# Performance work log

Hardware: AMD Instinct MI355X
Metric: run time of the kernel (lower is better)

Reference implementation:

```python
import jax, jax.numpy as jnp
import numpy as np

N = 50000      # nodes
E = 800000     # edges (before self loops)
D_IN = 128
HID = 64
HEADS = 8
D_OUT = 10


def setup_inputs() -> dict:
    key = jax.random.key(0)
    ks = jax.random.split(key, 16)
    sc = 0.05
    x = jax.random.normal(ks[0], (N, D_IN), dtype=jnp.float32)
    edge_index = jax.random.randint(ks[1], (2, E), 0, N, dtype=jnp.int64)
    return {
        "x": x,
        "edge_index": edge_index,
        "W1": jax.random.normal(ks[2], (HEADS * HID, D_IN), dtype=jnp.float32) * sc,
        "a1_src": jax.random.normal(ks[3], (HEADS, HID), dtype=jnp.float32) * sc,
        "a1_dst": jax.random.normal(ks[4], (HEADS, HID), dtype=jnp.float32) * sc,
        "b1": jnp.zeros((HEADS * HID,), jnp.float32),
        "W2": jax.random.normal(ks[5], (HID, HEADS * HID), dtype=jnp.float32) * sc,
        "a2_src": jax.random.normal(ks[6], (1, HID), dtype=jnp.float32) * sc,
        "a2_dst": jax.random.normal(ks[7], (1, HID), dtype=jnp.float32) * sc,
        "b2": jnp.zeros((HID,), jnp.float32),
        "W3": jax.random.normal(ks[8], (HID, HID), dtype=jnp.float32) * sc,
        "a3_src": jax.random.normal(ks[9], (1, HID), dtype=jnp.float32) * sc,
        "a3_dst": jax.random.normal(ks[10], (1, HID), dtype=jnp.float32) * sc,
        "b3": jnp.zeros((HID,), jnp.float32),
        "Wc": jax.random.normal(ks[11], (D_OUT, HID), dtype=jnp.float32) * sc,
        "bc": jnp.zeros((D_OUT,), jnp.float32),
    }


def gat_conv(x, src, dst, W, a_src, a_dst, b, concat):
    """PyG GATConv (eval mode, add_self_loops already applied to src/dst)."""
    heads, out_ch = a_src.shape
    n = x.shape[0]
    h = (x @ W.T).reshape(n, heads, out_ch)          # [N, H, C]
    a_s = jnp.einsum('nhc,hc->nh', h, a_src)          # [N, H]
    a_d = jnp.einsum('nhc,hc->nh', h, a_dst)          # [N, H]
    e = jax.nn.leaky_relu(a_s[src] + a_d[dst], 0.2)   # [Etot, H]
    # segment softmax over incoming edges of each destination node
    m = jax.ops.segment_max(e, dst, num_segments=n)
    ex = jnp.exp(e - m[dst])
    s = jax.ops.segment_sum(ex, dst, num_segments=n)
    alpha = ex / (s[dst] + 1e-16)                     # [Etot, H]
    out = jax.ops.segment_sum(h[src] * alpha[:, :, None], dst, num_segments=n)
    if concat:
        out = out.reshape(n, heads * out_ch)
    else:
        out = out.mean(axis=1)
    return out + b


def reference(x, edge_index, W1, a1_src, a1_dst, b1, W2, a2_src, a2_dst, b2,
              W3, a3_src, a3_dst, b3, Wc, bc):
    loops = jnp.arange(N, dtype=edge_index.dtype)
    src = jnp.concatenate([edge_index[0], loops])
    dst = jnp.concatenate([edge_index[1], loops])
    h = jax.nn.elu(gat_conv(x, src, dst, W1, a1_src, a1_dst, b1, True))
    h = jax.nn.elu(gat_conv(h, src, dst, W2, a2_src, a2_dst, b2, False))
    h = jax.nn.elu(gat_conv(h, src, dst, W3, a3_src, a3_dst, b3, False))
    return h @ Wc.T + bc
```

## Files before the change

### kernel.cpp

```cpp
#include <hip/hip_runtime.h>
#include <math.h>

#define N_NODES 50000
#define N_EDGES 800000
#define ETOT    (N_EDGES + N_NODES)
#define COL_CAP (ETOT + 3 * N_NODES + 64)

typedef short bf16x8 __attribute__((ext_vector_type(8)));
typedef float f32x4  __attribute__((ext_vector_type(4)));
typedef float f32x2  __attribute__((ext_vector_type(2)));

__device__ __forceinline__ float b2f(unsigned int u16) {
    return __uint_as_float(u16 << 16);
}
__device__ __forceinline__ unsigned short f2b(float f) {
    unsigned int u = __float_as_uint(f);
    u += 0x7fffu + ((u >> 16) & 1u);
    return (unsigned short)(u >> 16);
}

__global__ __launch_bounds__(256) void k_prep(const float* __restrict__ x,
                                              const float* __restrict__ w1,
                                              const float* __restrict__ w2,
                                              const float* __restrict__ w3,
                                              const float* __restrict__ a1s,
                                              const float* __restrict__ a1d,
                                              unsigned short* __restrict__ xb,
                                              unsigned short* __restrict__ o1,
                                              unsigned short* __restrict__ o2,
                                              unsigned short* __restrict__ o3,
                                              float* __restrict__ U,
                                              int* __restrict__ deg,
                                              int* __restrict__ flag) {
    int i = blockIdx.x * 256 + threadIdx.x;
    if (i < N_NODES) deg[i] = 0;
    if (i == 0) *flag = 0;
    if (blockIdx.x < 8) {
        int h = blockIdx.x;
        int which = threadIdx.x >> 7, k = threadIdx.x & 127;
        const float* av = which ? a1d : a1s;
        float acc = 0.f;
        for (int c = 0; c < 64; ++c)
            acc += av[h * 64 + c] * w1[(size_t)(h * 64 + c) * 128 + k];
        U[(which * 8 + h) * 128 + k] = acc;
    }
    if (i < 512 * 128 / 4) {
        float4 v = ((const float4*)w1)[i];
        ushort2* o = (ushort2*)(o1 + i * 4);
        o[0] = make_ushort2(f2b(v.x), f2b(v.y));
        o[1] = make_ushort2(f2b(v.z), f2b(v.w));
    }
    if (i < 64 * 512 / 4) {
        float4 v = ((const float4*)w2)[i];
        ushort2* o = (ushort2*)(o2 + i * 4);
        o[0] = make_ushort2(f2b(v.x), f2b(v.y));
        o[1] = make_ushort2(f2b(v.z), f2b(v.w));
    }
    if (i < 64 * 64 / 4) {
        float4 v = ((const float4*)w3)[i];
        ushort2* o = (ushort2*)(o3 + i * 4);
        o[0] = make_ushort2(f2b(v.x), f2b(v.y));
        o[1] = make_ushort2(f2b(v.z), f2b(v.w));
    }
    if (i < N_NODES * 128 / 8) {
        const float4* xp = (const float4*)x + (size_t)i * 2;
        float4 v0 = xp[0], v1 = xp[1];
        unsigned int u0 = (unsigned int)f2b(v0.x) | ((unsigned int)f2b(v0.y) << 16);
        unsigned int u1 = (unsigned int)f2b(v0.z) | ((unsigned int)f2b(v0.w) << 16);
        unsigned int u2 = (unsigned int)f2b(v1.x) | ((unsigned int)f2b(v1.y) << 16);
        unsigned int u3 = (unsigned int)f2b(v1.z) | ((unsigned int)f2b(v1.w) << 16);
        *(uint4*)(xb + (size_t)i * 8) = make_uint4(u0, u1, u2, u3);
    }
}

__global__ __launch_bounds__(256) void k_attn(const unsigned short* __restrict__ xb,
                                              const float* __restrict__ U,
                                              float* __restrict__ asrc,
                                              float* __restrict__ adst) {
    __shared__ float sU[16 * 132];
    __shared__ unsigned short sX[16 * 136];
    int t = threadIdx.x;
    for (int i = t; i < 2048; i += 256) sU[(i >> 7) * 132 + (i & 127)] = U[i];
    int n0 = blockIdx.x * 16;
    {
        int r = t >> 4, c = (t & 15) * 8;
        *(uint4*)&sX[r * 136 + c] = *(const uint4*)(xb + (size_t)(n0 + r) * 128 + c);
    }
    __syncthreads();
    int nl = t >> 4, o = t & 15;
    const unsigned short* xr = sX + nl * 136;
    const float* ur = sU + o * 132;
    float acc = 0.f;
#pragma unroll 8
    for (int k2 = 0; k2 < 128; ++k2) acc += b2f(xr[k2]) * ur[k2];
    int n = n0 + nl;
    if (o < 8) asrc[n * 8 + o] = acc;
    else       adst[n * 8 + (o - 8)] = acc;
}

__global__ void k_detect(const int* __restrict__ idx, int* __restrict__ flag) {
    int i = blockIdx.x * blockDim.x + threadIdx.x;
    int v = idx[2 * i + 1];
    unsigned long long any = __ballot(v != 0);
    if ((threadIdx.x & 63) == 0 && any) atomicOr(flag, 1);
}

__device__ __forceinline__ int edge_src(const int* idx, int e, int is32) {
    return is32 ? idx[e] : idx[2 * e];
}
__device__ __forceinline__ int edge_dst(const int* idx, int e, int is32) {
    return is32 ? idx[N_EDGES + e] : idx[2 * (N_EDGES + e)];
}

__global__ void k_degree(const int* __restrict__ idx, const int* __restrict__ flag,
                         int* __restrict__ deg) {
    int e = blockIdx.x * blockDim.x + threadIdx.x;
    if (e >= ETOT) return;
    int is32 = *flag;
    int d = (e < N_EDGES) ? edge_dst(idx, e, is32) : (e - N_EDGES);
    atomicAdd(&deg[d], 1);
}

__global__ __launch_bounds__(256) void k_scan1(const int* __restrict__ deg,
                                               int* __restrict__ rowptr,
                                               int* __restrict__ bsum) {
    __shared__ int sd[256];
    int t = threadIdx.x;
    int i = blockIdx.x * 256 + t;
    int v = (i < N_NODES) ? ((deg[i] + 3) & ~3) : 0;
    sd[t] = v;
    __syncthreads();
#pragma unroll
    for (int off = 1; off < 256; off <<= 1) {
        int a = (t >= off) ? sd[t - off] : 0;
        __syncthreads();
        sd[t] += a;
        __syncthreads();
    }
    if (i < N_NODES) rowptr[i] = sd[t] - v;
    if (t == 255) bsum[blockIdx.x] = sd[255];
}

__global__ __launch_bounds__(256) void k_scan2(int* __restrict__ bsum,
                                               int* __restrict__ boff,
                                               int* __restrict__ rowptr,
                                               int nb) {
    __shared__ int sd[256];
    int t = threadIdx.x;
    int v = (t < nb) ? bsum[t] : 0;
    sd[t] = v;
    __syncthreads();
#pragma unroll
    for (int off = 1; off < 256; off <<= 1) {
        int a = (t >= off) ? sd[t - off] : 0;
        __syncthreads();
        sd[t] += a;
        __syncthreads();
    }
    boff[t] = sd[t] - v;
    if (t == 255) rowptr[N_NODES] = sd[255];
}

__global__ __launch_bounds__(256) void k_scan3(int* __restrict__ rowptr,
                                               const int* __restrict__ boff,
                                               const int* __restrict__ deg,
                                               int* __restrict__ cursor,
                                               int* __restrict__ col) {
    int i = blockIdx.x * 256 + threadIdx.x;
    if (i == 0) {
        int tot = rowptr[N_NODES];
        for (int q = 0; q < 48; ++q) col[tot + q] = 0;
    }
    if (i >= N_NODES) return;
    int r = rowptr[i] + boff[blockIdx.x];
    rowptr[i] = r;
    cursor[i] = r;
    int d = deg[i];
    int pd = (d + 3) & ~3;
    for (int p = r + d; p < r + pd; ++p) col[p] = 0;
}

__global__ void k_scatter(const int* __restrict__ idx, const int* __restrict__ flag,
                          int* __restrict__ cursor, int* __restrict__ col) {
    int e = blockIdx.x * blockDim.x + threadIdx.x;
    if (e >= ETOT) return;
    int is32 = *flag;
    int s, d;
    if (e < N_EDGES) { s = edge_src(idx, e, is32); d = edge_dst(idx, e, is32); }
    else             { s = d = e - N_EDGES; }
    int pos = atomicAdd(&cursor[d], 1);
    col[pos] = s;
}

__device__ __forceinline__ void aggx_slot(int idx, int rem, float tt, unsigned int xx,
                                          float adn, float& ssum, f32x2* acc) {
    float e = tt + adn;
    e = fmaxf(e, 0.2f * e);
    float ex = __expf(e);
    ex = (idx < rem) ? ex : 0.f;
    ssum += ex;
    float fx = __uint_as_float(xx << 16);
    float fy = __uint_as_float(xx & 0xffff0000u);
    int exi = __float_as_int(ex);
#pragma unroll
    for (int hh = 0; hh < 8; ++hh) {
        float wh = __int_as_float(__builtin_amdgcn_readlane(exi, hh << 3));
        acc[hh].x = fmaf(fx, wh, acc[hh].x);
        acc[hh].y = fmaf(fy, wh, acc[hh].y);
    }
}

__global__ __launch_bounds__(256) void k_aggx(const unsigned short* __restrict__ xb,
                                              const float* __restrict__ asrc,
                                              const float* __restrict__ adst,
                                              const int* __restrict__ rowptr,
                                              const int* __restrict__ degv,
                                              const int* __restrict__ col,
                                              unsigned short* __restrict__ aggX) {
    int n = blockIdx.x * 4 + (threadIdx.x >> 6);
    if (n >= N_NODES) return;
    int l = threadIdx.x & 63;
    int j = l >> 3;
    unsigned lx2 = (unsigned)(l << 1);
    int start = rowptr[n];
    int end   = start + degv[n];
    float adn = adst[((unsigned)n << 3) + (unsigned)j];

    float ssum = 0.f;
    f32x2 acc[8];
#pragma unroll
    for (int hh = 0; hh < 8; ++hh) acc[hh] = (f32x2){0.f, 0.f};

    float tA0, tA1, tA2, tA3, tB0, tB1, tB2, tB3;
    unsigned int xA0, xA1, xA2, xA3, xB0, xB1, xB2, xB3;
    int4 cA, cB;

#define GATHX(c, T0, T1, T2, T3, X0, X1, X2, X3)                              \
    T0 = asrc[(((unsigned)(c).x) << 3) + (unsigned)j];                        \
    T1 = asrc[(((unsigned)(c).y) << 3) + (unsigned)j];                        \
    T2 = asrc[(((unsigned)(c).z) << 3) + (unsigned)j];                        \
    T3 = asrc[(((unsigned)(c).w) << 3) + (unsigned)j];                        \
    X0 = *(const unsigned int*)(xb + (((unsigned)(c).x) << 7) + lx2);         \
    X1 = *(const unsigned int*)(xb + (((unsigned)(c).y) << 7) + lx2);         \
    X2 = *(const unsigned int*)(xb + (((unsigned)(c).z) << 7) + lx2);         \
    X3 = *(const unsigned int*)(xb + (((unsigned)(c).w) << 7) + lx2);

    int k = start;
    cA = *(const int4*)(col + k);
    cB = *(const int4*)(col + k + 4);
    GATHX(cA, tA0, tA1, tA2, tA3, xA0, xA1, xA2, xA3);
    for (;;) {
        bool hasB = (k + 4 < end);
        if (hasB) {
            GATHX(cB, tB0, tB1, tB2, tB3, xB0, xB1, xB2, xB3);
            cA = *(const int4*)(col + k + 8);
        }
        {
            int rem = end - k;
            aggx_slot(0, rem, tA0, xA0, adn, ssum, acc);
            aggx_slot(1, rem, tA1, xA1, adn, ssum, acc);
            aggx_slot(2, rem, tA2, xA2, adn, ssum, acc);
            aggx_slot(3, rem, tA3, xA3, adn, ssum, acc);
        }
        k += 4;
        if (!hasB) break;
        bool hasA = (k + 4 < end);
        if (hasA) {
            GATHX(cA, tA0, tA1, tA2, tA3, xA0, xA1, xA2, xA3);
            cB = *(const int4*)(col + k + 8);
        }
        {
            int rem = end - k;
            aggx_slot(0, rem, tB0, xB0, adn, ssum, acc);
            aggx_slot(1, rem, tB1, xB1, adn, ssum, acc);
            aggx_slot(2, rem, tB2, xB2, adn, ssum, acc);
            aggx_slot(3, rem, tB3, xB3, adn, ssum, acc);
        }
        k += 4;
        if (!hasA) break;
    }
#undef GATHX

    size_t base = (size_t)n * 1024 + lx2;
#pragma unroll
    for (int hh = 0; hh < 8; ++hh) {
        float sh = __int_as_float(__builtin_amdgcn_readlane(__float_as_int(ssum), hh << 3));
        float iv = 1.f / (sh + 1e-16f);
        unsigned int lo = f2b(acc[hh].x * iv);
        unsigned int hi = f2b(acc[hh].y * iv);
        *(unsigned int*)(aggX + base + hh * 128) = lo | (hi << 16);
    }
}

__global__ __launch_bounds__(256) void k_gemm12(const unsigned short* __restrict__ aggX,
                                                const unsigned short* __restrict__ W1b,
                                                const float* __restrict__ b1,
                                                const unsigned short* __restrict__ W2b,
                                                const float* __restrict__ a2s,
                                                const float* __restrict__ a2d,
                                                unsigned short* __restrict__ h2,
                                                float* __restrict__ asb,
                                                float* __restrict__ adb) {
    __shared__ unsigned short As[64 * 40];
    __shared__ unsigned short Bs[64 * 40];
    __shared__ unsigned short X2s[64 * 520];
    __shared__ float red_s[4][64];
    __shared__ float red_d[4][64];
    int t = threadIdx.x;
    int w = t >> 6, l = t & 63;
    int quad = l >> 4, lm = l & 15;
    int m0 = blockIdx.x * 64;
    int lr = t >> 2;
    int lc = (t & 3) * 8;

    for (int h = 0; h < 8; ++h) {
        f32x4 acc[4];
#pragma unroll
        for (int r = 0; r < 4; ++r) acc[r] = (f32x4){0.f, 0.f, 0.f, 0.f};
        for (int k0 = 0; k0 < 128; k0 += 32) {
            int m = m0 + lr;
            uint4 av = make_uint4(0, 0, 0, 0);
            if (m < N_NODES) av = *(const uint4*)(aggX + (size_t)m * 1024 + h * 128 + k0 + lc);
            *(uint4*)&As[lr * 40 + lc] = av;
            uint4 bv = *(const uint4*)(W1b + (size_t)(h * 64 + lr) * 128 + k0 + lc);
            *(uint4*)&Bs[lr * 40 + lc] = bv;
            __syncthreads();
            bf16x8 bfrag = *(const bf16x8*)&Bs[(w * 16 + lm) * 40 + quad * 8];
#pragma unroll
            for (int r = 0; r < 4; ++r) {
                bf16x8 afrag = *(const bf16x8*)&As[(r * 16 + lm) * 40 + quad * 8];
                acc[r] = __builtin_amdgcn_mfma_f32_16x16x32_bf16(afrag, bfrag, acc[r], 0, 0, 0);
            }
            __syncthreads();
        }
        float bcol = b1[h * 64 + w * 16 + lm];
#pragma unroll
        for (int r = 0; r < 4; ++r)
#pragma unroll
            for (int g = 0; g < 4; ++g) {
                float v = acc[r][g] + bcol;
                v = (v > 0.f) ? v : expm1f(v);
                X2s[(r * 16 + quad * 4 + g) * 520 + h * 64 + w * 16 + lm] = f2b(v);
            }
    }
    __syncthreads();

    f32x4 acc[4];
#pragma unroll
    for (int r = 0; r < 4; ++r) acc[r] = (f32x4){0.f, 0.f, 0.f, 0.f};
    for (int k0 = 0; k0 < 512; k0 += 32) {
        uint4 bu = *(const uint4*)(W2b + (size_t)(w * 16 + lm) * 512 + k0 + quad * 8);
        bf16x8 bfrag = *(bf16x8*)&bu;
#pragma unroll
        for (int r = 0; r < 4; ++r) {
            bf16x8 afrag = *(const bf16x8*)&X2s[(r * 16 + lm) * 520 + k0 + quad * 8];
            acc[r] = __builtin_amdgcn_mfma_f32_16x16x32_bf16(afrag, bfrag, acc[r], 0, 0, 0);
        }
    }

#pragma unroll
    for (int r = 0; r < 4; ++r)
#pragma unroll
        for (int g = 0; g < 4; ++g) {
            int m = m0 + r * 16 + quad * 4 + g;
            if (m < N_NODES) h2[(size_t)m * 64 + w * 16 + lm] = f2b(acc[r][g]);
        }

    float as = a2s[w * 16 + lm];
    float ad = a2d[w * 16 + lm];
#pragma unroll
    for (int r = 0; r < 4; ++r) {
#pragma unroll
        for (int g = 0; g < 4; ++g) {
            float vs = acc[r][g] * as;
            float vd = acc[r][g] * ad;
#pragma unroll
            for (int off = 1; off < 16; off <<= 1) {
                vs += __shfl_xor(vs, off);
                vd += __shfl_xor(vd, off);
            }
            if (lm == 0) {
                red_s[w][r * 16 + quad * 4 + g] = vs;
                red_d[w][r * 16 + quad * 4 + g] = vd;
            }
        }
    }
    __syncthreads();
    if (t < 64) {
        float vs = red_s[0][t] + red_s[1][t] + red_s[2][t] + red_s[3][t];
        float vd = red_d[0][t] + red_d[1][t] + red_d[2][t] + red_d[3][t];
        int m = m0 + t;
        if (m < N_NODES) {
            asb[m] = vs;
            adb[m] = vd;
        }
    }
}

__global__ __launch_bounds__(256) void k_gemm(const unsigned short* __restrict__ Ab,
                                              const unsigned short* __restrict__ W,
                                              unsigned short* __restrict__ C,
                                              const float* __restrict__ a_src,
                                              const float* __restrict__ a_dst,
                                              float* __restrict__ asb,
                                              float* __restrict__ adb,
                                              int M, int K, int Nout) {
    __shared__ unsigned short As[64 * 40];
    __shared__ unsigned short Bs[64 * 40];
    __shared__ float red_s[4][64];
    __shared__ float red_d[4][64];
    int t = threadIdx.x;
    int w = t >> 6, l = t & 63;
    int quad = l >> 4, lm = l & 15;
    int m0 = blockIdx.y * 64, n0 = blockIdx.x * 64;
    int lr = t >> 2;
    int lc = (t & 3) * 8;

    f32x4 acc[4];
#pragma unroll
    for (int r = 0; r < 4; ++r) acc[r] = (f32x4){0.f, 0.f, 0.f, 0.f};

    for (int k0 = 0; k0 < K; k0 += 32) {
        int m = m0 + lr;
        uint4 av = make_uint4(0, 0, 0, 0);
        if (m < M) av = *(const uint4*)(Ab + (size_t)m * K + k0 + lc);
        *(uint4*)&As[lr * 40 + lc] = av;
        uint4 bv = *(const uint4*)(W + (size_t)(n0 + lr) * K + k0 + lc);
        *(uint4*)&Bs[lr * 40 + lc] = bv;
        __syncthreads();

        bf16x8 bfrag = *(const bf16x8*)&Bs[(w * 16 + lm) * 40 + quad * 8];
#pragma unroll
        for (int r = 0; r < 4; ++r) {
            bf16x8 afrag = *(const bf16x8*)&As[(r * 16 + lm) * 40 + quad * 8];
            acc[r] = __builtin_amdgcn_mfma_f32_16x16x32_bf16(afrag, bfrag, acc[r], 0, 0, 0);
        }
        __syncthreads();
    }

#pragma unroll
    for (int r = 0; r < 4; ++r)
#pragma unroll
        for (int g = 0; g < 4; ++g) {
            int m = m0 + r * 16 + quad * 4 + g;
            if (m < M) C[(size_t)m * Nout + n0 + w * 16 + lm] = f2b(acc[r][g]);
        }

    float as = a_src[w * 16 + lm];
    float ad = a_dst[w * 16 + lm];
#pragma unroll
    for (int r = 0; r < 4; ++r) {
#pragma unroll
        for (int g = 0; g < 4; ++g) {
            float vs = acc[r][g] * as;
            float vd = acc[r][g] * ad;
#pragma unroll
            for (int off = 1; off < 16; off <<= 1) {
                vs += __shfl_xor(vs, off);
                vd += __shfl_xor(vd, off);
            }
            if (lm == 0) {
                red_s[w][r * 16 + quad * 4 + g] = vs;
                red_d[w][r * 16 + quad * 4 + g] = vd;
            }
        }
    }
    __syncthreads();
    if (t < 64) {
        float vs = red_s[0][t] + red_s[1][t] + red_s[2][t] + red_s[3][t];
        float vd = red_d[0][t] + red_d[1][t] + red_d[2][t] + red_d[3][t];
        int m = m0 + t;
        if (m < M) {
            asb[m] = vs;
            adb[m] = vd;
        }
    }
}

__global__ __launch_bounds__(256) void k_agg1(const unsigned short* __restrict__ h,
                                              const float* __restrict__ asrc,
                                              const float* __restrict__ adst,
                                              const int* __restrict__ rowptr,
                                              const int* __restrict__ degv,
                                              const int* __restrict__ col,
                                              const float* __restrict__ bias,
                                              unsigned short* __restrict__ out) {
    int n = blockIdx.x * 4 + (threadIdx.x >> 6);
    if (n >= N_NODES) return;
    int l = threadIdx.x & 63;
    int start = rowptr[n];
    int end   = start + degv[n];
    float adn = adst[n];

    float ssum = 0.f, o = 0.f;
    float tA0, tA1, tA2, tA3, tB0, tB1, tB2, tB3;
    unsigned short qA0, qA1, qA2, qA3, qB0, qB1, qB2, qB3;
    int4 cA, cB;

#define GATH1(c, T0, T1, T2, T3, Q0, Q1, Q2, Q3)                              \
    T0 = asrc[(unsigned)(c).x];                                               \
    T1 = asrc[(unsigned)(c).y];                                               \
    T2 = asrc[(unsigned)(c).z];                                               \
    T3 = asrc[(unsigned)(c).w];                                               \
    Q0 = h[(((unsigned)(c).x) << 6) + (unsigned)l];                           \
    Q1 = h[(((unsigned)(c).y) << 6) + (unsigned)l];                           \
    Q2 = h[(((unsigned)(c).z) << 6) + (unsigned)l];                           \
    Q3 = h[(((unsigned)(c).w) << 6) + (unsigned)l];

#define ASLOT1(IDX, TT, QQ, rem)                                              \
    {                                                                         \
        float e = TT + adn;                                                   \
        e = fmaxf(e, 0.2f * e);                                               \
        float ex = __expf(e);                                                 \
        ex = ((IDX) < (rem)) ? ex : 0.f;                                      \
        ssum += ex;                                                           \
        o += ex * b2f(QQ);                                                    \
    }

    int k = start;
    cA = *(const int4*)(col + k);
    cB = *(const int4*)(col + k + 4);
    GATH1(cA, tA0, tA1, tA2, tA3, qA0, qA1, qA2, qA3);
    for (;;) {
        bool hasB = (k + 4 < end);
        if (hasB) {
            GATH1(cB, tB0, tB1, tB2, tB3, qB0, qB1, qB2, qB3);
            cA = *(const int4*)(col + k + 8);
        }
        {
            int rem = end - k;
            ASLOT1(0, tA0, qA0, rem);
            ASLOT1(1, tA1, qA1, rem);
            ASLOT1(2, tA2, qA2, rem);
            ASLOT1(3, tA3, qA3, rem);
        }
        k += 4;
        if (!hasB) break;
        bool hasA = (k + 4 < end);
        if (hasA) {
            GATH1(cA, tA0, tA1, tA2, tA3, qA0, qA1, qA2, qA3);
            cB = *(const int4*)(col + k + 8);
        }
        {
            int rem = end - k;
            ASLOT1(0, tB0, qB0, rem);
            ASLOT1(1, tB1, qB1, rem);
            ASLOT1(2, tB2, qB2, rem);
            ASLOT1(3, tB3, qB3, rem);
        }
        k += 4;
        if (!hasA) break;
    }
#undef GATH1
#undef ASLOT1

    float v = o / (ssum + 1e-16f) + bias[l];
    v = (v > 0.f) ? v : expm1f(v);
    out[(size_t)n * 64 + l] = f2b(v);
}

__global__ __launch_bounds__(256) void k_classifier(const unsigned short* __restrict__ h,
                                                    const float* __restrict__ Wc,
                                                    const float* __restrict__ bc,
                                                    float* __restrict__ out) {
    __shared__ float sW[640];
    for (int i = threadIdx.x; i < 640; i += blockDim.x) sW[i] = Wc[i];
    __syncthreads();
    int idx = blockIdx.x * blockDim.x + threadIdx.x;
    if (idx >= N_NODES * 10) return;
    int n = idx / 10, d = idx - n * 10;
    const unsigned short* hr = h + (size_t)n * 64;
    const float* wr = sW + d * 64;
    float acc = 0.f;
#pragma unroll
    for (int c = 0; c < 64; ++c) acc += b2f(hr[c]) * wr[c];
    out[idx] = acc + bc[d];
}

extern "C" void kernel_launch(void* const* d_in, const int* in_sizes, int n_in,
                              void* d_out, int out_size, void* d_ws, size_t ws_size,
                              hipStream_t stream) {
    const float* x    = (const float*)d_in[0];
    const int*   eidx = (const int*)  d_in[1];
    const float* W1   = (const float*)d_in[2];
    const float* a1s  = (const float*)d_in[3];
    const float* a1d  = (const float*)d_in[4];
    const float* b1   = (const float*)d_in[5];
    const float* W2   = (const float*)d_in[6];
    const float* a2s  = (const float*)d_in[7];
    const float* a2d  = (const float*)d_in[8];
    const float* b2   = (const float*)d_in[9];
    const float* W3   = (const float*)d_in[10];
    const float* a3s  = (const float*)d_in[11];
    const float* a3d  = (const float*)d_in[12];
    const float* b3   = (const float*)d_in[13];
    const float* Wc   = (const float*)d_in[14];
    const float* bc   = (const float*)d_in[15];
    float* out = (float*)d_out;

    float* asbuf = (float*)d_ws;
    float* adbuf = asbuf + (size_t)N_NODES * 8;
    unsigned short* aggX = (unsigned short*)(adbuf + (size_t)N_NODES * 8);
    unsigned short* h2  = aggX + (size_t)N_NODES * 1024;
    unsigned short* x3  = h2  + (size_t)N_NODES * 64;
    unsigned short* h3  = x3  + (size_t)N_NODES * 64;
    unsigned short* x4  = h3  + (size_t)N_NODES * 64;
    unsigned short* xb  = x4  + (size_t)N_NODES * 64;
    unsigned short* W1b = xb  + (size_t)N_NODES * 128;
    unsigned short* W2b = W1b + 512 * 128;
    unsigned short* W3b = W2b + 64 * 512;
    float* U    = (float*)(W3b + 64 * 64);
    int* ibase  = (int*)(U + 16 * 128);
    int* deg    = ibase;
    int* flag   = deg + N_NODES;
    int* rowptr = flag + 1;
    int* cursor = rowptr + N_NODES + 1;
    int* bsum   = cursor + N_NODES;
    int* boff   = bsum + 256;
    int* col    = boff + 256;

    dim3 blk(256);
    const int SCAN_BLOCKS = (N_NODES + 255) / 256;
    const int PREP_BLOCKS = (N_NODES * 128 / 8 + 255) / 256;

    k_prep<<<PREP_BLOCKS, blk, 0, stream>>>(x, W1, W2, W3, a1s, a1d,
                                            xb, W1b, W2b, W3b, U, deg, flag);
    k_attn<<<N_NODES / 16, blk, 0, stream>>>(xb, U, asbuf, adbuf);

    k_detect<<<32, blk, 0, stream>>>(eidx, flag);
    k_degree<<<(ETOT + 255) / 256, blk, 0, stream>>>(eidx, flag, deg);
    k_scan1<<<SCAN_BLOCKS, blk, 0, stream>>>(deg, rowptr, bsum);
    k_scan2<<<1, blk, 0, stream>>>(bsum, boff, rowptr, SCAN_BLOCKS);
    k_scan3<<<SCAN_BLOCKS, blk, 0, stream>>>(rowptr, boff, deg, cursor, col);
    k_scatter<<<(ETOT + 255) / 256, blk, 0, stream>>>(eidx, flag, cursor, col);

    int mblocks = (N_NODES + 63) / 64;
    int nblocks = N_NODES / 4;

    k_aggx<<<nblocks, blk, 0, stream>>>(xb, asbuf, adbuf, rowptr, deg, col, aggX);

    k_gemm12<<<mblocks, blk, 0, stream>>>(aggX, W1b, b1, W2b, a2s, a2d,
                                          h2, asbuf, adbuf);

    k_agg1<<<nblocks, blk, 0, stream>>>(h2, asbuf, adbuf, rowptr, deg, col, b2, x3);

    k_gemm<<<dim3(1, mblocks), blk, 0, stream>>>(x3, W3b, h3,
                                                 a3s, a3d, asbuf, adbuf,
                                                 N_NODES, 64, 64);
    k_agg1<<<nblocks, blk, 0, stream>>>(h3, asbuf, adbuf, rowptr, deg, col, b3, x4);

    k_classifier<<<(N_NODES * 10 + 255) / 256, blk, 0, stream>>>(x4, Wc, bc, out);
}
```

Measured before the change: 437.1 us.

## Restructure fused layer-1/2 GEMM: one wave per head, direct-register operand loads

The fused GEMM kernel now launches 512 threads (8 waves). Each wave computes one attention head's 64x64 layer-1 tile, loading A and B fragments straight from global memory into registers. This removes the serial 8-head loop with its shared-memory staging and syncs. The second GEMM splits the 64x64 output across 8 waves as 16x32 tiles, and the attention-score reduction is changed to match. The cost is higher register pressure from the 16 accumulators per wave and uncoalesced fragment loads from global memory.

```diff
diff --git a/kernel.cpp b/kernel.cpp
--- a/kernel.cpp
+++ b/kernel.cpp
@@ -292,103 +292,111 @@
     }
 }
 
-__global__ __launch_bounds__(256) void k_gemm12(const unsigned short* __restrict__ aggX,
-                                                const unsigned short* __restrict__ W1b,
-                                                const float* __restrict__ b1,
-                                                const unsigned short* __restrict__ W2b,
-                                                const float* __restrict__ a2s,
-                                                const float* __restrict__ a2d,
-                                                unsigned short* __restrict__ h2,
-                                                float* __restrict__ asb,
-                                                float* __restrict__ adb) {
-    __shared__ unsigned short As[64 * 40];
-    __shared__ unsigned short Bs[64 * 40];
+__global__ __launch_bounds__(512, 4) void k_gemm12(const unsigned short* __restrict__ aggX,
+                                                   const unsigned short* __restrict__ W1b,
+                                                   const float* __restrict__ b1,
+                                                   const unsigned short* __restrict__ W2b,
+                                                   const float* __restrict__ a2s,
+                                                   const float* __restrict__ a2d,
+                                                   unsigned short* __restrict__ h2,
+                                                   float* __restrict__ asb,
+                                                   float* __restrict__ adb) {
     __shared__ unsigned short X2s[64 * 520];
-    __shared__ float red_s[4][64];
-    __shared__ float red_d[4][64];
+    __shared__ float red_s[8][16];
+    __shared__ float red_d[8][16];
     int t = threadIdx.x;
     int w = t >> 6, l = t & 63;
     int quad = l >> 4, lm = l & 15;
     int m0 = blockIdx.x * 64;
-    int lr = t >> 2;
-    int lc = (t & 3) * 8;
-
-    for (int h = 0; h < 8; ++h) {
-        f32x4 acc[4];
-#pragma unroll
-        for (int r = 0; r < 4; ++r) acc[r] = (f32x4){0.f, 0.f, 0.f, 0.f};
-        for (int k0 = 0; k0 < 128; k0 += 32) {
-            int m = m0 + lr;
-            uint4 av = make_uint4(0, 0, 0, 0);
-            if (m < N_NODES) av = *(const uint4*)(aggX + (size_t)m * 1024 + h * 128 + k0 + lc);
-            *(uint4*)&As[lr * 40 + lc] = av;
-            uint4 bv = *(const uint4*)(W1b + (size_t)(h * 64 + lr) * 128 + k0 + lc);
-            *(uint4*)&Bs[lr * 40 + lc] = bv;
-            __syncthreads();
-            bf16x8 bfrag = *(const bf16x8*)&Bs[(w * 16 + lm) * 40 + quad * 8];
-#pragma unroll
-            for (int r = 0; r < 4; ++r) {
-                bf16x8 afrag = *(const bf16x8*)&As[(r * 16 + lm) * 40 + quad * 8];
-                acc[r] = __builtin_amdgcn_mfma_f32_16x16x32_bf16(afrag, bfrag, acc[r], 0, 0, 0);
+
+    {
+        int h = w;
+        f32x4 acc1[4][4];
+#pragma unroll
+        for (int rt = 0; rt < 4; ++rt)
+#pragma unroll
+            for (int ct = 0; ct < 4; ++ct) acc1[rt][ct] = (f32x4){0.f, 0.f, 0.f, 0.f};
+
+#pragma unroll
+        for (int k0 = 0; k0 < 4; ++k0) {
+            bf16x8 af[4];
+#pragma unroll
+            for (int rt = 0; rt < 4; ++rt) {
+                int m = m0 + rt * 16 + lm;
+                uint4 au = make_uint4(0, 0, 0, 0);
+                if (m < N_NODES)
+                    au = *(const uint4*)(aggX + (size_t)m * 1024 + h * 128 + k0 * 32 + quad * 8);
+                af[rt] = *(bf16x8*)&au;
             }
-            __syncthreads();
-        }
-        float bcol = b1[h * 64 + w * 16 + lm];
-#pragma unroll
-        for (int r = 0; r < 4; ++r)
-#pragma unroll
-            for (int g = 0; g < 4; ++g) {
-                float v = acc[r][g] + bcol;
-                v = (v > 0.f) ? v : expm1f(v);
-                X2s[(r * 16 + quad * 4 + g) * 520 + h * 64 + w * 16 + lm] = f2b(v);
+#pragma unroll
+            for (int ct = 0; ct < 4; ++ct) {
+                uint4 bu = *(const uint4*)(W1b + (size_t)(h * 64 + ct * 16 + lm) * 128 + k0 * 32 + quad * 8);
+                bf16x8 bf_ = *(bf16x8*)&bu;
+#pragma unroll
+                for (int rt = 0; rt < 4; ++rt)
+                    acc1[rt][ct] = __builtin_amdgcn_mfma_f32_16x16x32_bf16(af[rt], bf_, acc1[rt][ct], 0, 0, 0);
             }
+        }
+#pragma unroll
+        for (int ct = 0; ct < 4; ++ct) {
+            float bcol = b1[h * 64 + ct * 16 + lm];
+#pragma unroll
+            for (int rt = 0; rt < 4; ++rt)
+#pragma unroll
+                for (int g = 0; g < 4; ++g) {
+                    float v = acc1[rt][ct][g] + bcol;
+                    v = (v > 0.f) ? v : expm1f(v);
+                    X2s[(rt * 16 + quad * 4 + g) * 520 + h * 64 + ct * 16 + lm] = f2b(v);
+                }
+        }
     }
     __syncthreads();
 
-    f32x4 acc[4];
-#pragma unroll
-    for (int r = 0; r < 4; ++r) acc[r] = (f32x4){0.f, 0.f, 0.f, 0.f};
+    int rt2 = w >> 1;
+    int ct0 = (w & 1) * 2, ct1 = ct0 + 1;
+    f32x4 acc2a = (f32x4){0.f, 0.f, 0.f, 0.f};
+    f32x4 acc2b = (f32x4){0.f, 0.f, 0.f, 0.f};
+#pragma unroll 4
     for (int k0 = 0; k0 < 512; k0 += 32) {
-        uint4 bu = *(const uint4*)(W2b + (size_t)(w * 16 + lm) * 512 + k0 + quad * 8);
-        bf16x8 bfrag = *(bf16x8*)&bu;
-#pragma unroll
-        for (int r = 0; r < 4; ++r) {
-            bf16x8 afrag = *(const bf16x8*)&X2s[(r * 16 + lm) * 520 + k0 + quad * 8];
-            acc[r] = __builtin_amdgcn_mfma_f32_16x16x32_bf16(afrag, bfrag, acc[r], 0, 0, 0);
-        }
-    }
-
-#pragma unroll
-    for (int r = 0; r < 4; ++r)
+        bf16x8 af = *(const bf16x8*)&X2s[(rt2 * 16 + lm) * 520 + k0 + quad * 8];
+        uint4 b0 = *(const uint4*)(W2b + (size_t)(ct0 * 16 + lm) * 512 + k0 + quad * 8);
+        uint4 b1u = *(const uint4*)(W2b + (size_t)(ct1 * 16 + lm) * 512 + k0 + quad * 8);
+        acc2a = __builtin_amdgcn_mfma_f32_16x16x32_bf16(af, *(bf16x8*)&b0, acc2a, 0, 0, 0);
+        acc2b = __builtin_amdgcn_mfma_f32_16x16x32_bf16(af, *(bf16x8*)&b1u, acc2b, 0, 0, 0);
+    }
+
+#pragma unroll
+    for (int g = 0; g < 4; ++g) {
+        int m = m0 + rt2 * 16 + quad * 4 + g;
+        if (m < N_NODES) {
+            h2[(size_t)m * 64 + ct0 * 16 + lm] = f2b(acc2a[g]);
+            h2[(size_t)m * 64 + ct1 * 16 + lm] = f2b(acc2b[g]);
+        }
+    }
+
+    {
+        float as0 = a2s[ct0 * 16 + lm], ad0 = a2d[ct0 * 16 + lm];
+        float as1 = a2s[ct1 * 16 + lm], ad1 = a2d[ct1 * 16 + lm];
 #pragma unroll
         for (int g = 0; g < 4; ++g) {
-            int m = m0 + r * 16 + quad * 4 + g;
-            if (m < N_NODES) h2[(size_t)m * 64 + w * 16 + lm] = f2b(acc[r][g]);
-        }
-
-    float as = a2s[w * 16 + lm];
-    float ad = a2d[w * 16 + lm];
-#pragma unroll
-    for (int r = 0; r < 4; ++r) {
-#pragma unroll
-        for (int g = 0; g < 4; ++g) {
-            float vs = acc[r][g] * as;
-            float vd = acc[r][g] * ad;
+            float vs = acc2a[g] * as0 + acc2b[g] * as1;
+            float vd = acc2a[g] * ad0 + acc2b[g] * ad1;
 #pragma unroll
             for (int off = 1; off < 16; off <<= 1) {
                 vs += __shfl_xor(vs, off);
                 vd += __shfl_xor(vd, off);
             }
             if (lm == 0) {
-                red_s[w][r * 16 + quad * 4 + g] = vs;
-                red_d[w][r * 16 + quad * 4 + g] = vd;
+                red_s[w][quad * 4 + g] = vs;
+                red_d[w][quad * 4 + g] = vd;
             }
         }
     }
     __syncthreads();
     if (t < 64) {
-        float vs = red_s[0][t] + red_s[1][t] + red_s[2][t] + red_s[3][t];
-        float vd = red_d[0][t] + red_d[1][t] + red_d[2][t] + red_d[3][t];
+        int rt = t >> 4, rr = t & 15;
+        float vs = red_s[2 * rt][rr] + red_s[2 * rt + 1][rr];
+        float vd = red_d[2 * rt][rr] + red_d[2 * rt + 1][rr];
         int m = m0 + t;
         if (m < N_NODES) {
             asb[m] = vs;
@@ -639,8 +647,8 @@
 
     k_aggx<<<nblocks, blk, 0, stream>>>(xb, asbuf, adbuf, rowptr, deg, col, aggX);
 
-    k_gemm12<<<mblocks, blk, 0, stream>>>(aggX, W1b, b1, W2b, a2s, a2d,
-                                          h2, asbuf, adbuf);
+    k_gemm12<<<mblocks, dim3(512), 0, stream>>>(aggX, W1b, b1, W2b, a2s, a2d,
+                                                h2, asbuf, adbuf);
 
     k_agg1<<<nblocks, blk, 0, stream>>>(h2, asbuf, adbuf, rowptr, deg, col, b2, x3);
 
```

After: 436.9 us. About the same (-0.0%).
